# Optimization experiments

Hardware: AMD Instinct MI355X
Metric: run time of the kernel (lower is better)

## Reference

```python
import jax, jax.numpy as jnp
import numpy as np

V, D, C, H = 32, 128, 2048, 8
B, M = 8, 2048
HD = D // H


def rms_norm(x, scale):
    # Whole-tensor (per-batch) RMS over dims (1,2), as in the source (quirky but faithful).
    Bx, Mx, Dx = x.shape
    fr = jnp.sqrt(jnp.sum(x * x, axis=(1, 2))) * (Mx * Dx) ** -0.5  # (B,)
    raw = x / fr[:, None, None]
    return scale[:Mx, :][None, :, :] * raw


def rope_tables(Mx):
    i = jnp.arange(D // 2, dtype=jnp.float32)
    # NOTE: faithful to source: exponent uses (i-1), not i.
    base = jnp.power(10000.0, -2.0 * (i - 1.0) / D)  # (D/2,)
    pos = jnp.arange(Mx, dtype=jnp.float32)
    ang = pos[:, None] * base[None, :]  # (M, D/2)
    return jnp.cos(ang), jnp.sin(ang)


def apply_rope(t, cos, sin):
    # Equivalent to bmm with the block-diagonal 2x2 rotation matrices:
    # out[2i]   =  t[2i]*cos + t[2i+1]*sin
    # out[2i+1] = -t[2i]*sin + t[2i+1]*cos
    te, to = t[..., 0::2], t[..., 1::2]
    oe = te * cos + to * sin
    oo = -te * sin + to * cos
    return jnp.stack([oe, oo], axis=-1).reshape(t.shape)


def mha(q, k, v, in_w, in_b, out_w, out_b):
    Bx, Mx, _ = q.shape
    qp = q @ in_w[:D].T + in_b[:D]
    kp = k @ in_w[D:2 * D].T + in_b[D:2 * D]
    vp = v @ in_w[2 * D:].T + in_b[2 * D:]
    qh = qp.reshape(Bx, Mx, H, HD).transpose(0, 2, 1, 3)
    kh = kp.reshape(Bx, Mx, H, HD).transpose(0, 2, 1, 3)
    vh = vp.reshape(Bx, Mx, H, HD).transpose(0, 2, 1, 3)
    scores = jnp.einsum('bhqd,bhkd->bhqk', qh, kh) / jnp.sqrt(jnp.float32(HD))
    causal = jnp.tril(jnp.ones((Mx, Mx), dtype=bool))
    scores = jnp.where(causal[None, None], scores, -jnp.inf)
    probs = jax.nn.softmax(scores, axis=-1)  # dropout=0.1 in train mode; eval here
    o = jnp.einsum('bhqk,bhkd->bhqd', probs, vh)
    o = o.transpose(0, 2, 1, 3).reshape(Bx, Mx, D)
    return o @ out_w.T + out_b


def setup_inputs():
    key = jax.random.key(0)
    ks = jax.random.split(key, 12)
    s = 0.02
    return {
        'idx': jax.random.randint(ks[0], (B, M), 0, V),
        'targets': jax.random.randint(ks[1], (B, M), 0, V),
        'emb': jax.random.normal(ks[2], (V, D), jnp.float32) * s,
        'rms_scale': jnp.ones((C, D), jnp.float32),
        'Wq': jax.random.normal(ks[3], (D, D), jnp.float32) * s,
        'Wk': jax.random.normal(ks[4], (D, D), jnp.float32) * s,
        'Wv': jax.random.normal(ks[5], (D, D), jnp.float32) * s,
        'in_proj_w': jax.random.normal(ks[6], (3 * D, D), jnp.float32) * s,
        'in_proj_b': jnp.zeros((3 * D,), jnp.float32),
        'out_proj_w': jax.random.normal(ks[7], (D, D), jnp.float32) * s,
        'out_proj_b': jnp.zeros((D,), jnp.float32),
        'lin_w': jax.random.normal(ks[8], (D, D), jnp.float32) * s,
        'lin_b': jnp.zeros((D,), jnp.float32),
        'out_w': jax.random.normal(ks[9], (V, D), jnp.float32) * s,
        'out_b': jnp.zeros((V,), jnp.float32),
    }


def reference(idx, targets, emb, rms_scale, Wq, Wk, Wv, in_proj_w, in_proj_b,
              out_proj_w, out_proj_b, lin_w, lin_b, out_w, out_b):
    x = emb[idx]                                  # (B, M, D)
    x = rms_norm(x, rms_scale)
    Q = x @ Wq.T
    K = x @ Wk.T
    Vv = x @ Wv.T
    cos, sin = rope_tables(x.shape[1])
    q_out = apply_rope(Q, cos, sin)
    k_out = apply_rope(K, cos, sin)
    v_out = apply_rope(Vv, cos, sin)              # source rotates V too (faithful)
    x = x + mha(q_out, k_out, v_out, in_proj_w, in_proj_b, out_proj_w, out_proj_b)
    x = rms_norm(x, rms_scale)
    x = x + jax.nn.relu(x @ lin_w.T + lin_b)
    logits = x @ out_w.T + out_b                  # (B, M, V)
    logp = jax.nn.log_softmax(logits, axis=-1)
    nll = -jnp.take_along_axis(logp, targets[..., None], axis=-1)[..., 0]
    loss = jnp.mean(nll)
    return logits, loss
```

## Files before the change

kernel.cpp:

```cpp
#include <hip/hip_runtime.h>
#include <hip/hip_bf16.h>
#include <math.h>

#define Vv   32
#define Dd   128
#define Hh   8
#define Bb   8
#define Mm   2048
#define BM   (Bb*Mm)
#define NEL  (BM*Dd)
#define XNS  140
#define QKS  396

typedef _Float16 half4_t __attribute__((ext_vector_type(4)));
typedef _Float16 half8_t __attribute__((ext_vector_type(8)));
typedef __fp16   fp16x2  __attribute__((ext_vector_type(2)));
typedef float    float4_t __attribute__((ext_vector_type(4)));
#define MFMA16 __builtin_amdgcn_mfma_f32_16x16x16f16
#define MFMA32 __builtin_amdgcn_mfma_f32_16x16x32_f16

#if __has_builtin(__builtin_amdgcn_exp2f)
__device__ __forceinline__ float fexp2(float x) { return __builtin_amdgcn_exp2f(x); }
#else
__device__ __forceinline__ float fexp2(float x) { return __expf(x * 0.6931471805599453f); }
#endif

__global__ __launch_bounds__(256) void front_kernel(const float* __restrict__ Wq,
                                                    const float* __restrict__ Wk,
                                                    const float* __restrict__ Wv,
                                                    const float* __restrict__ in_w,
                                                    const float* __restrict__ out_pw,
                                                    const float* __restrict__ lin_w,
                                                    const float* __restrict__ out_w,
                                                    _Float16* __restrict__ Wh,
                                                    float* __restrict__ cosT,
                                                    float* __restrict__ sinT,
                                                    const int* __restrict__ idx,
                                                    const float* __restrict__ emb,
                                                    _Float16* __restrict__ Xh,
                                                    float* __restrict__ partials,
                                                    float* __restrict__ lossOut) {
    __shared__ float wsum[4];
    if (blockIdx.x < 1040) {
        if (blockIdx.x == 0 && threadIdx.x == 0) lossOut[0] = 0.f;
        int gid = blockIdx.x * 256 + threadIdx.x;
        if (gid < 135168) {
            const float* src;
            int i;
            if (gid < 131072) {
                int seg = gid >> 14; i = gid & 16383;
                src = seg == 0 ? Wq : seg == 1 ? Wk : seg == 2 ? Wv :
                      seg < 6 ? in_w + (size_t)(seg - 3) * 16384 :
                      seg == 6 ? out_pw : lin_w;
            } else { src = out_w; i = gid - 131072; }
            int tile = i >> 8, within = i & 255;
            int nt = tile >> 3, kk = tile & 7;
            int r = within >> 4, cc = within & 15;
            Wh[gid] = (_Float16)src[(nt * 16 + r) * 128 + kk * 16 + cc];
        } else {
            int rid = gid - 135168;
            int i = rid & 63, m = rid >> 6;
            float ex = -2.0f * ((float)i - 1.0f) / 128.0f;
            float basef = expf(ex * 9.210340371976184f);
            float ang = (float)m * basef;
            cosT[rid] = cosf(ang);
            sinT[rid] = sinf(ang);
        }
    } else {
        int blk = blockIdx.x - 1040;
        int gid = blk * 256 + threadIdx.x;
        int token = gid >> 5, t4 = gid & 31;
        float4 x = *(const float4*)(emb + (size_t)idx[token] * 128 + t4 * 4);
        half4_t o;
        o[0] = (_Float16)x.x; o[1] = (_Float16)x.y; o[2] = (_Float16)x.z; o[3] = (_Float16)x.w;
        *(half4_t*)(Xh + (size_t)gid * 4) = o;
        float v = x.x * x.x + x.y * x.y + x.z * x.z + x.w * x.w;
        #pragma unroll
        for (int off = 32; off; off >>= 1) v += __shfl_xor(v, off);
        int lane = threadIdx.x & 63, wave = threadIdx.x >> 6;
        if (lane == 0) wsum[wave] = v;
        __syncthreads();
        if (threadIdx.x == 0) partials[blk] = wsum[0] + wsum[1] + wsum[2] + wsum[3];
    }
}

__global__ __launch_bounds__(512, 4) void gemm_qkvproj_kernel(const _Float16* __restrict__ xh,
                                                              const float* __restrict__ scale,
                                                              const float* __restrict__ part1,
                                                              const _Float16* __restrict__ Whqkv,
                                                              const _Float16* __restrict__ Whin,
                                                              const float* __restrict__ in_b,
                                                              const float* __restrict__ cosT,
                                                              const float* __restrict__ sinT,
                                                              _Float16* __restrict__ xnh,
                                                              _Float16* __restrict__ Qp,
                                                              _Float16* __restrict__ Kp,
                                                              _Float16* __restrict__ Vp) {
    __shared__ _Float16 xn[32 * XNS];
    __shared__ _Float16 qkv[32 * QKS];
    __shared__ float wsum0[8];
    int tid = threadIdx.x;
    int row0 = blockIdx.x * 32;
    {
        float v = (tid < 256) ? part1[(row0 >> 11) * 256 + tid] : 0.f;
        #pragma unroll
        for (int off = 32; off; off >>= 1) v += __shfl_xor(v, off);
        if ((tid & 63) == 0) wsum0[tid >> 6] = v;
    }
    __syncthreads();
    float iv = 512.0f / sqrtf(((wsum0[0] + wsum0[1]) + (wsum0[2] + wsum0[3])) +
                              ((wsum0[4] + wsum0[5]) + (wsum0[6] + wsum0[7])));
    {
        int rw = tid >> 4, c8 = (tid & 15) * 8;
        int m = (row0 + rw) & (Mm - 1);
        half8_t x8 = *(const half8_t*)(xh + (size_t)(row0 + rw) * 128 + c8);
        const float* sp = scale + (size_t)m * 128 + c8;
        float4 s0 = *(const float4*)sp;
        float4 s1 = *(const float4*)(sp + 4);
        half8_t o8;
        o8[0] = (_Float16)((float)x8[0] * iv * s0.x);
        o8[1] = (_Float16)((float)x8[1] * iv * s0.y);
        o8[2] = (_Float16)((float)x8[2] * iv * s0.z);
        o8[3] = (_Float16)((float)x8[3] * iv * s0.w);
        o8[4] = (_Float16)((float)x8[4] * iv * s1.x);
        o8[5] = (_Float16)((float)x8[5] * iv * s1.y);
        o8[6] = (_Float16)((float)x8[6] * iv * s1.z);
        o8[7] = (_Float16)((float)x8[7] * iv * s1.w);
        *(half8_t*)(xn + rw * XNS + c8) = o8;
        *(half8_t*)(xnh + (size_t)(row0 + rw) * 128 + c8) = o8;
    }
    __syncthreads();
    int wave = tid >> 6, lane = tid & 63;
    int r = lane & 15, c = lane >> 4;
    int nb = wave * 48;
    int aoff = c * 8;
    int boff = r * 16 + (c & 1) * 8;
    int bsel = c >> 1;
    {
        float4_t acc[2][3];
        #pragma unroll
        for (int rt = 0; rt < 2; rt++)
            #pragma unroll
            for (int t = 0; t < 3; t++) acc[rt][t] = (float4_t){0.f, 0.f, 0.f, 0.f};
        #pragma unroll
        for (int kk = 0; kk < 4; kk++) {
            half8_t a0 = *(const half8_t*)(xn + r * XNS + kk * 32 + aoff);
            half8_t a1 = *(const half8_t*)(xn + (16 + r) * XNS + kk * 32 + aoff);
            half8_t wf[3];
            #pragma unroll
            for (int t = 0; t < 3; t++)
                wf[t] = *(const half8_t*)(Whqkv + ((wave * 3 + t) * 8 + kk * 2 + bsel) * 256 + boff);
            #pragma unroll
            for (int t = 0; t < 3; t++) {
                acc[0][t] = MFMA32(a0, wf[t], acc[0][t], 0, 0, 0);
                acc[1][t] = MFMA32(a1, wf[t], acc[1][t], 0, 0, 0);
            }
        }
        #pragma unroll
        for (int rt = 0; rt < 2; rt++) {
            #pragma unroll
            for (int t = 0; t < 3; t++) {
                int n = nb + t * 16 + r;
                int ci = (n & 127) >> 1;
                #pragma unroll
                for (int reg = 0; reg < 4; reg++) {
                    int m2 = (row0 + rt * 16 + 4 * c + reg) & (Mm - 1);
                    float v = acc[rt][t][reg];
                    float vp = __shfl_xor(v, 1);
                    float cs = cosT[m2 * 64 + ci], sn = sinT[m2 * 64 + ci];
                    v = (n & 1) ? (-vp * sn + v * cs) : (v * cs + vp * sn);
                    qkv[(rt * 16 + 4 * c + reg) * QKS + n] = (_Float16)v;
                }
            }
        }
    }
    __syncthreads();
    {
        int seg_lo = nb >> 7;
        int seg_hi = (nb + 32) >> 7;
        float4_t acc[2][3];
        #pragma unroll
        for (int rt = 0; rt < 2; rt++)
            #pragma unroll
            for (int t = 0; t < 3; t++) acc[rt][t] = (float4_t){0.f, 0.f, 0.f, 0.f};
        #pragma unroll
        for (int kk = 0; kk < 4; kk++) {
            half8_t al0 = *(const half8_t*)(qkv + r * QKS + seg_lo * 128 + kk * 32 + aoff);
            half8_t al1 = *(const half8_t*)(qkv + (16 + r) * QKS + seg_lo * 128 + kk * 32 + aoff);
            half8_t ah0 = *(const half8_t*)(qkv + r * QKS + seg_hi * 128 + kk * 32 + aoff);
            half8_t ah1 = *(const half8_t*)(qkv + (16 + r) * QKS + seg_hi * 128 + kk * 32 + aoff);
            #pragma unroll
            for (int t = 0; t < 3; t++) {
                int colg = nb + t * 16;
                int seg = colg >> 7;
                int ntl = (colg & 127) >> 4;
                half8_t wf = *(const half8_t*)(Whin + ((seg * 8 + ntl) * 8 + kk * 2 + bsel) * 256 + boff);
                bool lo = (seg == seg_lo);
                acc[0][t] = MFMA32(lo ? al0 : ah0, wf, acc[0][t], 0, 0, 0);
                acc[1][t] = MFMA32(lo ? al1 : ah1, wf, acc[1][t], 0, 0, 0);
            }
        }
        int bb = row0 >> 11;
        #pragma unroll
        for (int rt = 0; rt < 2; rt++) {
            int t16 = ((row0 + rt * 16) & 2047) >> 4;
            #pragma unroll
            for (int t = 0; t < 3; t++) {
                int colg = nb + t * 16;
                int seg = colg >> 7;
                int h = (colg & 127) >> 4;
                size_t tb = ((size_t)(bb * 8 + h) * 128 + t16) * 256;
                float bv = in_b[colg + r];
                _Float16* dst = seg == 0 ? Qp : seg == 1 ? Kp : Vp;
                #pragma unroll
                for (int reg = 0; reg < 4; reg++) {
                    float v = acc[rt][t][reg] + bv;
                    int key = 4 * c + reg;
                    if (seg < 2) dst[tb + key * 16 + r] = (_Float16)v;
                    else         dst[tb + r * 16 + key] = (_Float16)v;
                }
            }
        }
    }
}

__global__ __launch_bounds__(512, 4) void gemm_ep1_kernel(const _Float16* __restrict__ Oh,
                                                          const _Float16* __restrict__ W6,
                                                          const float* __restrict__ bias,
                                                          const _Float16* __restrict__ xnh,
                                                          _Float16* __restrict__ xresh,
                                                          float* __restrict__ partials) {
    __shared__ _Float16 At[32 * XNS];
    int tid = threadIdx.x;
    int row0 = blockIdx.x * 32;
    {
        int rw = tid >> 4, c8 = (tid & 15) * 8;
        *(half8_t*)(At + rw * XNS + c8) = *(const half8_t*)(Oh + (size_t)(row0 + rw) * 128 + c8);
    }
    __syncthreads();
    int wave = tid >> 6, lane = tid & 63;
    int r = lane & 15, c = lane >> 4;
    int aoff = c * 8;
    int boff = r * 16 + (c & 1) * 8;
    int bsel = c >> 1;
    int n0 = wave * 16;
    float4_t acc[2];
    acc[0] = (float4_t){0.f, 0.f, 0.f, 0.f};
    acc[1] = (float4_t){0.f, 0.f, 0.f, 0.f};
    #pragma unroll
    for (int kk = 0; kk < 4; kk++) {
        half8_t a0 = *(const half8_t*)(At + r * XNS + kk * 32 + aoff);
        half8_t a1 = *(const half8_t*)(At + (16 + r) * XNS + kk * 32 + aoff);
        half8_t wf = *(const half8_t*)(W6 + (wave * 8 + kk * 2 + bsel) * 256 + boff);
        acc[0] = MFMA32(a0, wf, acc[0], 0, 0, 0);
        acc[1] = MFMA32(a1, wf, acc[1], 0, 0, 0);
    }
    float lssq = 0.f;
    int n = n0 + r;
    float bv = bias[n];
    #pragma unroll
    for (int rt = 0; rt < 2; rt++) {
        #pragma unroll
        for (int reg = 0; reg < 4; reg++) {
            int row = row0 + rt * 16 + 4 * c + reg;
            float v = acc[rt][reg] + bv + (float)xnh[(size_t)row * 128 + n];
            lssq += v * v;
            xresh[(size_t)row * 128 + n] = (_Float16)v;
        }
    }
    #pragma unroll
    for (int off = 32; off; off >>= 1) lssq += __shfl_xor(lssq, off);
    __shared__ float wsum[8];
    if (lane == 0) wsum[wave] = lssq;
    __syncthreads();
    if (tid == 0) partials[blockIdx.x] = ((wsum[0] + wsum[1]) + (wsum[2] + wsum[3])) +
                                        ((wsum[4] + wsum[5]) + (wsum[6] + wsum[7]));
}

__global__ __launch_bounds__(512, 4) void gemm_ep2_kernel(const _Float16* __restrict__ xresh,
                                                          const float* __restrict__ scale,
                                                          const float* __restrict__ part2,
                                                          const _Float16* __restrict__ W7,
                                                          const float* __restrict__ bias,
                                                          _Float16* __restrict__ ffoh) {
    __shared__ _Float16 At[32 * XNS];
    int tid = threadIdx.x;
    int row0 = blockIdx.x * 32;
    float pv = part2[(row0 >> 11) * 64 + (tid & 63)];
    #pragma unroll
    for (int off = 32; off; off >>= 1) pv += __shfl_xor(pv, off);
    float iv = 512.0f / sqrtf(pv);
    {
        int rw = tid >> 4, c8 = (tid & 15) * 8;
        int m = (row0 + rw) & (Mm - 1);
        half8_t x8 = *(const half8_t*)(xresh + (size_t)(row0 + rw) * 128 + c8);
        const float* sp = scale + (size_t)m * 128 + c8;
        float4 s0 = *(const float4*)sp;
        float4 s1 = *(const float4*)(sp + 4);
        half8_t o8;
        o8[0] = (_Float16)((float)x8[0] * iv * s0.x);
        o8[1] = (_Float16)((float)x8[1] * iv * s0.y);
        o8[2] = (_Float16)((float)x8[2] * iv * s0.z);
        o8[3] = (_Float16)((float)x8[3] * iv * s0.w);
        o8[4] = (_Float16)((float)x8[4] * iv * s1.x);
        o8[5] = (_Float16)((float)x8[5] * iv * s1.y);
        o8[6] = (_Float16)((float)x8[6] * iv * s1.z);
        o8[7] = (_Float16)((float)x8[7] * iv * s1.w);
        *(half8_t*)(At + rw * XNS + c8) = o8;
    }
    __syncthreads();
    int wave = tid >> 6, lane = tid & 63;
    int r = lane & 15, c = lane >> 4;
    int aoff = c * 8;
    int boff = r * 16 + (c & 1) * 8;
    int bsel = c >> 1;
    int n0 = wave * 16;
    float4_t acc[2];
    acc[0] = (float4_t){0.f, 0.f, 0.f, 0.f};
    acc[1] = (float4_t){0.f, 0.f, 0.f, 0.f};
    #pragma unroll
    for (int kk = 0; kk < 4; kk++) {
        half8_t a0 = *(const half8_t*)(At + r * XNS + kk * 32 + aoff);
        half8_t a1 = *(const half8_t*)(At + (16 + r) * XNS + kk * 32 + aoff);
        half8_t wf = *(const half8_t*)(W7 + (wave * 8 + kk * 2 + bsel) * 256 + boff);
        acc[0] = MFMA32(a0, wf, acc[0], 0, 0, 0);
        acc[1] = MFMA32(a1, wf, acc[1], 0, 0, 0);
    }
    int n = n0 + r;
    float bv = bias[n];
    #pragma unroll
    for (int rt = 0; rt < 2; rt++) {
        #pragma unroll
        for (int reg = 0; reg < 4; reg++) {
            int row = row0 + rt * 16 + 4 * c + reg;
            float v = fmaxf(acc[rt][reg] + bv, 0.f) + (float)xresh[(size_t)row * 128 + n];
            ffoh[(size_t)row * 128 + n] = (_Float16)v;
        }
    }
}

__device__ __forceinline__ half4_t attn_exps(float4_t st, float& ls) {
    float p0 = fexp2(st[0]), p1 = fexp2(st[1]);
    float p2 = fexp2(st[2]), p3 = fexp2(st[3]);
    ls += (p0 + p1) + (p2 + p3);
    fp16x2 lo = __builtin_amdgcn_cvt_pkrtz(p0, p1);
    fp16x2 hi = __builtin_amdgcn_cvt_pkrtz(p2, p3);
    half4_t pf;
    pf[0] = (_Float16)lo[0]; pf[1] = (_Float16)lo[1];
    pf[2] = (_Float16)hi[0]; pf[3] = (_Float16)hi[1];
    return pf;
}
__device__ __forceinline__ half4_t attn_exps_masked(float4_t st, float& ls, int r, int c) {
    float p0 = (4 * c + 0 <= r) ? fexp2(st[0]) : 0.f;
    float p1 = (4 * c + 1 <= r) ? fexp2(st[1]) : 0.f;
    float p2 = (4 * c + 2 <= r) ? fexp2(st[2]) : 0.f;
    float p3 = (4 * c + 3 <= r) ? fexp2(st[3]) : 0.f;
    ls += (p0 + p1) + (p2 + p3);
    fp16x2 lo = __builtin_amdgcn_cvt_pkrtz(p0, p1);
    fp16x2 hi = __builtin_amdgcn_cvt_pkrtz(p2, p3);
    half4_t pf;
    pf[0] = (_Float16)lo[0]; pf[1] = (_Float16)lo[1];
    pf[2] = (_Float16)hi[0]; pf[3] = (_Float16)hi[1];
    return pf;
}

__global__ __launch_bounds__(256) void attn_kernel(const _Float16* __restrict__ Qp,
                                                   const _Float16* __restrict__ Kp,
                                                   const _Float16* __restrict__ Vp,
                                                   _Float16* __restrict__ Oh) {
    __shared__ float mrg[2][10][64];
    int wave = threadIdx.x >> 6, lane = threadIdx.x & 63;
    int pair = blockIdx.x * 2 + (wave >> 1);
    int split = wave & 1;
    int qa = pair & 63, bh = pair >> 6, qb = 127 - qa;
    int r = lane & 15, c = lane >> 4;
    int lofs = r * 16 + 4 * c;
    const _Float16* Kb = Kp + (size_t)bh * 32768 + lofs;
    const _Float16* Vb = Vp + (size_t)bh * 32768 + lofs;
    const _Float16* Qb = Qp + (size_t)bh * 32768 + lofs;
    half4_t qfa = *(const half4_t*)(Qb + qa * 256);
    half4_t qfb = *(const half4_t*)(Qb + qb * 256);
    const _Float16 qscale = (_Float16)0.36067376f;
    qfa *= qscale;
    qfb *= qscale;
    float4_t zero = {0.f, 0.f, 0.f, 0.f};
    float4_t oa = zero, ob = zero;
    float lsa = 0.f, lsb = 0.f;

    for (int kt = split; kt < qa; kt += 2) {
        half4_t k0 = *(const half4_t*)(Kb + (size_t)kt * 256);
        half4_t v0 = *(const half4_t*)(Vb + (size_t)kt * 256);
        float4_t sa = MFMA16(k0, qfa, zero, 0, 0, 0);
        float4_t sb = MFMA16(k0, qfb, zero, 0, 0, 0);
        half4_t pa = attn_exps(sa, lsa);
        half4_t pb = attn_exps(sb, lsb);
        oa = MFMA16(pa, v0, oa, 0, 0, 0);
        ob = MFMA16(pb, v0, ob, 0, 0, 0);
    }
    if ((qa & 1) == split) {
        half4_t k0 = *(const half4_t*)(Kb + (size_t)qa * 256);
        half4_t v0 = *(const half4_t*)(Vb + (size_t)qa * 256);
        float4_t sa = MFMA16(k0, qfa, zero, 0, 0, 0);
        float4_t sb = MFMA16(k0, qfb, zero, 0, 0, 0);
        half4_t pa = attn_exps_masked(sa, lsa, r, c);
        half4_t pb = attn_exps(sb, lsb);
        oa = MFMA16(pa, v0, oa, 0, 0, 0);
        ob = MFMA16(pb, v0, ob, 0, 0, 0);
    }
    {
        int s = qa + 1;
        if ((s & 1) != split) s++;
        for (int kt = s; kt < qb; kt += 2) {
            half4_t k0 = *(const half4_t*)(Kb + (size_t)kt * 256);
            half4_t v0 = *(const half4_t*)(Vb + (size_t)kt * 256);
            float4_t sb = MFMA16(k0, qfb, zero, 0, 0, 0);
            half4_t pb = attn_exps(sb, lsb);
            ob = MFMA16(pb, v0, ob, 0, 0, 0);
        }
    }
    if ((qb & 1) == split) {
        half4_t k0 = *(const half4_t*)(Kb + (size_t)qb * 256);
        half4_t v0 = *(const half4_t*)(Vb + (size_t)qb * 256);
        float4_t sb = MFMA16(k0, qfb, zero, 0, 0, 0);
        half4_t pb = attn_exps_masked(sb, lsb, r, c);
        ob = MFMA16(pb, v0, ob, 0, 0, 0);
    }
    int pib = wave >> 1;
    if (split == 1) {
        #pragma unroll
        for (int i = 0; i < 4; i++) {
            mrg[pib][i][lane] = oa[i];
            mrg[pib][4 + i][lane] = ob[i];
        }
        mrg[pib][8][lane] = lsa;
        mrg[pib][9][lane] = lsb;
    }
    __syncthreads();
    if (split == 0) {
        #pragma unroll
        for (int i = 0; i < 4; i++) {
            oa[i] += mrg[pib][i][lane];
            ob[i] += mrg[pib][4 + i][lane];
        }
        lsa += mrg[pib][8][lane];
        lsb += mrg[pib][9][lane];
        lsa += __shfl_xor(lsa, 16); lsa += __shfl_xor(lsa, 32);
        lsb += __shfl_xor(lsb, 16); lsb += __shfl_xor(lsb, 32);
        int b = bh >> 3, h = bh & 7;
        #pragma unroll
        for (int reg = 0; reg < 4; reg++) {
            float la = __shfl(lsa, 4 * c + reg);
            float lb = __shfl(lsb, 4 * c + reg);
            Oh[(size_t)(b * Mm + qa * 16 + 4 * c + reg) * 128 + h * 16 + r] = (_Float16)(oa[reg] / la);
            Oh[(size_t)(b * Mm + qb * 16 + 4 * c + reg) * 128 + h * 16 + r] = (_Float16)(ob[reg] / lb);
        }
    }
}

__global__ __launch_bounds__(256) void logits_loss_kernel(const _Float16* __restrict__ Xh,
                                                          const _Float16* __restrict__ Wo16,
                                                          const float* __restrict__ bo,
                                                          const int* __restrict__ targets,
                                                          float* __restrict__ logits,
                                                          float* __restrict__ lossOut) {
    __shared__ _Float16 At[64 * XNS];
    __shared__ float wn[4];
    int tid = threadIdx.x;
    int rowb = blockIdx.x * 64;
    #pragma unroll
    for (int it = 0; it < 4; it++) {
        int idx = tid + it * 256;
        int rw = idx >> 4, c8 = (idx & 15) * 8;
        *(half8_t*)(At + rw * XNS + c8) = *(const half8_t*)(Xh + (size_t)(rowb + rw) * 128 + c8);
    }
    __syncthreads();
    int wave = tid >> 6, lane = tid & 63;
    int r = lane & 15, c = lane >> 4;
    int aoff = c * 8;
    int boff = r * 16 + (c & 1) * 8;
    int bsel = c >> 1;
    int row0 = rowb + wave * 16;
    half8_t af[4];
    #pragma unroll
    for (int kk = 0; kk < 4; kk++)
        af[kk] = *(const half8_t*)(At + (wave * 16 + r) * XNS + kk * 32 + aoff);
    float4_t acc[2];
    acc[0] = (float4_t){0.f, 0.f, 0.f, 0.f};
    acc[1] = (float4_t){0.f, 0.f, 0.f, 0.f};
    #pragma unroll
    for (int kk = 0; kk < 4; kk++) {
        #pragma unroll
        for (int t = 0; t < 2; t++) {
            half8_t wf = *(const half8_t*)(Wo16 + (t * 8 + kk * 2 + bsel) * 256 + boff);
            acc[t] = MFMA32(af[kk], wf, acc[t], 0, 0, 0);
        }
    }
    float b0 = bo[r], b1 = bo[r + 16];
    float nll_s = 0.f;
    #pragma unroll
    for (int reg = 0; reg < 4; reg++) {
        int row = row0 + 4 * c + reg;
        float l0 = acc[0][reg] + b0;
        float l1 = acc[1][reg] + b1;
        logits[(size_t)row * 32 + r] = l0;
        logits[(size_t)row * 32 + 16 + r] = l1;
        float mx = fmaxf(l0, l1);
        #pragma unroll
        for (int off = 8; off; off >>= 1) mx = fmaxf(mx, __shfl_xor(mx, off));
        float se = __expf(l0 - mx) + __expf(l1 - mx);
        #pragma unroll
        for (int off = 8; off; off >>= 1) se += __shfl_xor(se, off);
        int tgt = targets[row];
        float sel = (tgt & 16) ? l1 : l0;
        float tval = __shfl(sel, (lane & 48) | (tgt & 15));
        nll_s += logf(se) + mx - tval;
    }
    nll_s += __shfl_xor(nll_s, 16);
    nll_s += __shfl_xor(nll_s, 32);
    if (lane == 0) wn[wave] = nll_s;
    __syncthreads();
    if (tid == 0) atomicAdd(lossOut, ((wn[0] + wn[1]) + (wn[2] + wn[3])) * (1.0f / (float)BM));
}

extern "C" void kernel_launch(void* const* d_in, const int* in_sizes, int n_in,
                              void* d_out, int out_size, void* d_ws, size_t ws_size,
                              hipStream_t stream) {
    const int*   idx       = (const int*)d_in[0];
    const int*   targets   = (const int*)d_in[1];
    const float* emb       = (const float*)d_in[2];
    const float* rms_scale = (const float*)d_in[3];
    const float* Wq        = (const float*)d_in[4];
    const float* Wk        = (const float*)d_in[5];
    const float* Wv        = (const float*)d_in[6];
    const float* in_w      = (const float*)d_in[7];
    const float* in_b      = (const float*)d_in[8];
    const float* out_pw    = (const float*)d_in[9];
    const float* out_pb    = (const float*)d_in[10];
    const float* lin_w     = (const float*)d_in[11];
    const float* lin_b     = (const float*)d_in[12];
    const float* out_w     = (const float*)d_in[13];
    const float* out_b     = (const float*)d_in[14];
    float* out = (float*)d_out;
    float* lossOut = out + (size_t)BM * Vv;

    char* base = (char*)d_ws;
    const size_t MB = 1024 * 1024;
    _Float16* xh16  = (_Float16*)base;
    _Float16* xnh   = (_Float16*)(base + 4 * MB);
    _Float16* Oh    = (_Float16*)(base + 8 * MB);
    _Float16* xresh = (_Float16*)(base + 12 * MB);
    _Float16* ffoh  = (_Float16*)(base + 16 * MB);
    _Float16* Qp    = (_Float16*)(base + 20 * MB);
    _Float16* Kp    = (_Float16*)(base + 24 * MB);
    _Float16* Vp    = (_Float16*)(base + 28 * MB);
    float*    cosT  = (float*)(base + 32 * MB);
    float*    sinT  = cosT + Mm * 64;
    float*    part1 = sinT + Mm * 64;
    float*    part2 = part1 + 2048;
    _Float16* Wh    = (_Float16*)(part2 + 512);

    front_kernel<<<1040 + 2048, 256, 0, stream>>>(Wq, Wk, Wv, in_w, out_pw, lin_w, out_w,
                                                  Wh, cosT, sinT, idx, emb, xh16, part1, lossOut);

    gemm_qkvproj_kernel<<<BM / 32, 512, 0, stream>>>(xh16, rms_scale, part1,
                                                     Wh, Wh + 3 * 16384, in_b,
                                                     cosT, sinT, xnh, Qp, Kp, Vp);

    attn_kernel<<<4096 / 2, 256, 0, stream>>>(Qp, Kp, Vp, Oh);

    gemm_ep1_kernel<<<BM / 32, 512, 0, stream>>>(Oh, Wh + 6 * 16384, out_pb, xnh, xresh, part2);
    gemm_ep2_kernel<<<BM / 32, 512, 0, stream>>>(xresh, rms_scale, part2, Wh + 7 * 16384, lin_b, ffoh);

    logits_loss_kernel<<<BM / 64, 256, 0, stream>>>(ffoh, Wh + 131072, out_b, targets, out, lossOut);
}
```

Measured before the change: 154.6 us.

## Merge all stages into one persistent kernel with software grid barriers

Replaces the six separate launches (front, qkv projection, attention, two epilogue GEMMs, logits/loss) with a single persistent kernel of 256 blocks. The stages are separated by atomic grid-wide barriers, and each block loops over several row tiles. This removes per-launch overhead and the gaps between kernels, and the final loss reduction becomes deterministic instead of using atomics. The cost is lower occupancy and parallelism in each stage, since only 256 blocks are resident. It also relies on all blocks being co-resident, and the barrier has a spin timeout that could silently break ordering.

```diff
diff --git a/kernel.cpp b/kernel.cpp
--- a/kernel.cpp
+++ b/kernel.cpp
@@ -11,6 +11,7 @@
 #define NEL  (BM*Dd)
 #define XNS  140
 #define QKS  396
+#define NBLK 256
 
 typedef _Float16 half4_t __attribute__((ext_vector_type(4)));
 typedef _Float16 half8_t __attribute__((ext_vector_type(8)));
@@ -25,318 +26,29 @@
 __device__ __forceinline__ float fexp2(float x) { return __expf(x * 0.6931471805599453f); }
 #endif
 
-__global__ __launch_bounds__(256) void front_kernel(const float* __restrict__ Wq,
-                                                    const float* __restrict__ Wk,
-                                                    const float* __restrict__ Wv,
-                                                    const float* __restrict__ in_w,
-                                                    const float* __restrict__ out_pw,
-                                                    const float* __restrict__ lin_w,
-                                                    const float* __restrict__ out_w,
-                                                    _Float16* __restrict__ Wh,
-                                                    float* __restrict__ cosT,
-                                                    float* __restrict__ sinT,
-                                                    const int* __restrict__ idx,
-                                                    const float* __restrict__ emb,
-                                                    _Float16* __restrict__ Xh,
-                                                    float* __restrict__ partials,
-                                                    float* __restrict__ lossOut) {
-    __shared__ float wsum[4];
-    if (blockIdx.x < 1040) {
-        if (blockIdx.x == 0 && threadIdx.x == 0) lossOut[0] = 0.f;
-        int gid = blockIdx.x * 256 + threadIdx.x;
-        if (gid < 135168) {
-            const float* src;
-            int i;
-            if (gid < 131072) {
-                int seg = gid >> 14; i = gid & 16383;
-                src = seg == 0 ? Wq : seg == 1 ? Wk : seg == 2 ? Wv :
-                      seg < 6 ? in_w + (size_t)(seg - 3) * 16384 :
-                      seg == 6 ? out_pw : lin_w;
-            } else { src = out_w; i = gid - 131072; }
-            int tile = i >> 8, within = i & 255;
-            int nt = tile >> 3, kk = tile & 7;
-            int r = within >> 4, cc = within & 15;
-            Wh[gid] = (_Float16)src[(nt * 16 + r) * 128 + kk * 16 + cc];
+__device__ __forceinline__ void grid_bar(unsigned* cnt, unsigned* gen) {
+    __syncthreads();
+    if (threadIdx.x == 0) {
+        __threadfence();
+        unsigned g = __hip_atomic_load(gen, __ATOMIC_RELAXED, __HIP_MEMORY_SCOPE_AGENT);
+        unsigned a = __hip_atomic_fetch_add(cnt, 1u, __ATOMIC_ACQ_REL, __HIP_MEMORY_SCOPE_AGENT) + 1u;
+        if (a == (unsigned)NBLK) {
+            __hip_atomic_store(cnt, 0u, __ATOMIC_RELAXED, __HIP_MEMORY_SCOPE_AGENT);
+            __hip_atomic_fetch_add(gen, 1u, __ATOMIC_RELEASE, __HIP_MEMORY_SCOPE_AGENT);
         } else {
-            int rid = gid - 135168;
-            int i = rid & 63, m = rid >> 6;
-            float ex = -2.0f * ((float)i - 1.0f) / 128.0f;
-            float basef = expf(ex * 9.210340371976184f);
-            float ang = (float)m * basef;
-            cosT[rid] = cosf(ang);
-            sinT[rid] = sinf(ang);
-        }
-    } else {
-        int blk = blockIdx.x - 1040;
-        int gid = blk * 256 + threadIdx.x;
-        int token = gid >> 5, t4 = gid & 31;
-        float4 x = *(const float4*)(emb + (size_t)idx[token] * 128 + t4 * 4);
-        half4_t o;
-        o[0] = (_Float16)x.x; o[1] = (_Float16)x.y; o[2] = (_Float16)x.z; o[3] = (_Float16)x.w;
-        *(half4_t*)(Xh + (size_t)gid * 4) = o;
-        float v = x.x * x.x + x.y * x.y + x.z * x.z + x.w * x.w;
-        #pragma unroll
-        for (int off = 32; off; off >>= 1) v += __shfl_xor(v, off);
-        int lane = threadIdx.x & 63, wave = threadIdx.x >> 6;
-        if (lane == 0) wsum[wave] = v;
-        __syncthreads();
-        if (threadIdx.x == 0) partials[blk] = wsum[0] + wsum[1] + wsum[2] + wsum[3];
-    }
+            int spins = 0;
+            while (__hip_atomic_load(gen, __ATOMIC_ACQUIRE, __HIP_MEMORY_SCOPE_AGENT) == g) {
+                __builtin_amdgcn_s_sleep(2);
+                if (++spins > (1 << 19)) break;
+            }
+        }
+        __threadfence();
+    }
+    __syncthreads();
 }
 
-__global__ __launch_bounds__(512, 4) void gemm_qkvproj_kernel(const _Float16* __restrict__ xh,
-                                                              const float* __restrict__ scale,
-                                                              const float* __restrict__ part1,
-                                                              const _Float16* __restrict__ Whqkv,
-                                                              const _Float16* __restrict__ Whin,
-                                                              const float* __restrict__ in_b,
-                                                              const float* __restrict__ cosT,
-                                                              const float* __restrict__ sinT,
-                                                              _Float16* __restrict__ xnh,
-                                                              _Float16* __restrict__ Qp,
-                                                              _Float16* __restrict__ Kp,
-                                                              _Float16* __restrict__ Vp) {
-    __shared__ _Float16 xn[32 * XNS];
-    __shared__ _Float16 qkv[32 * QKS];
-    __shared__ float wsum0[8];
-    int tid = threadIdx.x;
-    int row0 = blockIdx.x * 32;
-    {
-        float v = (tid < 256) ? part1[(row0 >> 11) * 256 + tid] : 0.f;
-        #pragma unroll
-        for (int off = 32; off; off >>= 1) v += __shfl_xor(v, off);
-        if ((tid & 63) == 0) wsum0[tid >> 6] = v;
-    }
-    __syncthreads();
-    float iv = 512.0f / sqrtf(((wsum0[0] + wsum0[1]) + (wsum0[2] + wsum0[3])) +
-                              ((wsum0[4] + wsum0[5]) + (wsum0[6] + wsum0[7])));
-    {
-        int rw = tid >> 4, c8 = (tid & 15) * 8;
-        int m = (row0 + rw) & (Mm - 1);
-        half8_t x8 = *(const half8_t*)(xh + (size_t)(row0 + rw) * 128 + c8);
-        const float* sp = scale + (size_t)m * 128 + c8;
-        float4 s0 = *(const float4*)sp;
-        float4 s1 = *(const float4*)(sp + 4);
-        half8_t o8;
-        o8[0] = (_Float16)((float)x8[0] * iv * s0.x);
-        o8[1] = (_Float16)((float)x8[1] * iv * s0.y);
-        o8[2] = (_Float16)((float)x8[2] * iv * s0.z);
-        o8[3] = (_Float16)((float)x8[3] * iv * s0.w);
-        o8[4] = (_Float16)((float)x8[4] * iv * s1.x);
-        o8[5] = (_Float16)((float)x8[5] * iv * s1.y);
-        o8[6] = (_Float16)((float)x8[6] * iv * s1.z);
-        o8[7] = (_Float16)((float)x8[7] * iv * s1.w);
-        *(half8_t*)(xn + rw * XNS + c8) = o8;
-        *(half8_t*)(xnh + (size_t)(row0 + rw) * 128 + c8) = o8;
-    }
-    __syncthreads();
-    int wave = tid >> 6, lane = tid & 63;
-    int r = lane & 15, c = lane >> 4;
-    int nb = wave * 48;
-    int aoff = c * 8;
-    int boff = r * 16 + (c & 1) * 8;
-    int bsel = c >> 1;
-    {
-        float4_t acc[2][3];
-        #pragma unroll
-        for (int rt = 0; rt < 2; rt++)
-            #pragma unroll
-            for (int t = 0; t < 3; t++) acc[rt][t] = (float4_t){0.f, 0.f, 0.f, 0.f};
-        #pragma unroll
-        for (int kk = 0; kk < 4; kk++) {
-            half8_t a0 = *(const half8_t*)(xn + r * XNS + kk * 32 + aoff);
-            half8_t a1 = *(const half8_t*)(xn + (16 + r) * XNS + kk * 32 + aoff);
-            half8_t wf[3];
-            #pragma unroll
-            for (int t = 0; t < 3; t++)
-                wf[t] = *(const half8_t*)(Whqkv + ((wave * 3 + t) * 8 + kk * 2 + bsel) * 256 + boff);
-            #pragma unroll
-            for (int t = 0; t < 3; t++) {
-                acc[0][t] = MFMA32(a0, wf[t], acc[0][t], 0, 0, 0);
-                acc[1][t] = MFMA32(a1, wf[t], acc[1][t], 0, 0, 0);
-            }
-        }
-        #pragma unroll
-        for (int rt = 0; rt < 2; rt++) {
-            #pragma unroll
-            for (int t = 0; t < 3; t++) {
-                int n = nb + t * 16 + r;
-                int ci = (n & 127) >> 1;
-                #pragma unroll
-                for (int reg = 0; reg < 4; reg++) {
-                    int m2 = (row0 + rt * 16 + 4 * c + reg) & (Mm - 1);
-                    float v = acc[rt][t][reg];
-                    float vp = __shfl_xor(v, 1);
-                    float cs = cosT[m2 * 64 + ci], sn = sinT[m2 * 64 + ci];
-                    v = (n & 1) ? (-vp * sn + v * cs) : (v * cs + vp * sn);
-                    qkv[(rt * 16 + 4 * c + reg) * QKS + n] = (_Float16)v;
-                }
-            }
-        }
-    }
-    __syncthreads();
-    {
-        int seg_lo = nb >> 7;
-        int seg_hi = (nb + 32) >> 7;
-        float4_t acc[2][3];
-        #pragma unroll
-        for (int rt = 0; rt < 2; rt++)
-            #pragma unroll
-            for (int t = 0; t < 3; t++) acc[rt][t] = (float4_t){0.f, 0.f, 0.f, 0.f};
-        #pragma unroll
-        for (int kk = 0; kk < 4; kk++) {
-            half8_t al0 = *(const half8_t*)(qkv + r * QKS + seg_lo * 128 + kk * 32 + aoff);
-            half8_t al1 = *(const half8_t*)(qkv + (16 + r) * QKS + seg_lo * 128 + kk * 32 + aoff);
-            half8_t ah0 = *(const half8_t*)(qkv + r * QKS + seg_hi * 128 + kk * 32 + aoff);
-            half8_t ah1 = *(const half8_t*)(qkv + (16 + r) * QKS + seg_hi * 128 + kk * 32 + aoff);
-            #pragma unroll
-            for (int t = 0; t < 3; t++) {
-                int colg = nb + t * 16;
-                int seg = colg >> 7;
-                int ntl = (colg & 127) >> 4;
-                half8_t wf = *(const half8_t*)(Whin + ((seg * 8 + ntl) * 8 + kk * 2 + bsel) * 256 + boff);
-                bool lo = (seg == seg_lo);
-                acc[0][t] = MFMA32(lo ? al0 : ah0, wf, acc[0][t], 0, 0, 0);
-                acc[1][t] = MFMA32(lo ? al1 : ah1, wf, acc[1][t], 0, 0, 0);
-            }
-        }
-        int bb = row0 >> 11;
-        #pragma unroll
-        for (int rt = 0; rt < 2; rt++) {
-            int t16 = ((row0 + rt * 16) & 2047) >> 4;
-            #pragma unroll
-            for (int t = 0; t < 3; t++) {
-                int colg = nb + t * 16;
-                int seg = colg >> 7;
-                int h = (colg & 127) >> 4;
-                size_t tb = ((size_t)(bb * 8 + h) * 128 + t16) * 256;
-                float bv = in_b[colg + r];
-                _Float16* dst = seg == 0 ? Qp : seg == 1 ? Kp : Vp;
-                #pragma unroll
-                for (int reg = 0; reg < 4; reg++) {
-                    float v = acc[rt][t][reg] + bv;
-                    int key = 4 * c + reg;
-                    if (seg < 2) dst[tb + key * 16 + r] = (_Float16)v;
-                    else         dst[tb + r * 16 + key] = (_Float16)v;
-                }
-            }
-        }
-    }
-}
-
-__global__ __launch_bounds__(512, 4) void gemm_ep1_kernel(const _Float16* __restrict__ Oh,
-                                                          const _Float16* __restrict__ W6,
-                                                          const float* __restrict__ bias,
-                                                          const _Float16* __restrict__ xnh,
-                                                          _Float16* __restrict__ xresh,
-                                                          float* __restrict__ partials) {
-    __shared__ _Float16 At[32 * XNS];
-    int tid = threadIdx.x;
-    int row0 = blockIdx.x * 32;
-    {
-        int rw = tid >> 4, c8 = (tid & 15) * 8;
-        *(half8_t*)(At + rw * XNS + c8) = *(const half8_t*)(Oh + (size_t)(row0 + rw) * 128 + c8);
-    }
-    __syncthreads();
-    int wave = tid >> 6, lane = tid & 63;
-    int r = lane & 15, c = lane >> 4;
-    int aoff = c * 8;
-    int boff = r * 16 + (c & 1) * 8;
-    int bsel = c >> 1;
-    int n0 = wave * 16;
-    float4_t acc[2];
-    acc[0] = (float4_t){0.f, 0.f, 0.f, 0.f};
-    acc[1] = (float4_t){0.f, 0.f, 0.f, 0.f};
-    #pragma unroll
-    for (int kk = 0; kk < 4; kk++) {
-        half8_t a0 = *(const half8_t*)(At + r * XNS + kk * 32 + aoff);
-        half8_t a1 = *(const half8_t*)(At + (16 + r) * XNS + kk * 32 + aoff);
-        half8_t wf = *(const half8_t*)(W6 + (wave * 8 + kk * 2 + bsel) * 256 + boff);
-        acc[0] = MFMA32(a0, wf, acc[0], 0, 0, 0);
-        acc[1] = MFMA32(a1, wf, acc[1], 0, 0, 0);
-    }
-    float lssq = 0.f;
-    int n = n0 + r;
-    float bv = bias[n];
-    #pragma unroll
-    for (int rt = 0; rt < 2; rt++) {
-        #pragma unroll
-        for (int reg = 0; reg < 4; reg++) {
-            int row = row0 + rt * 16 + 4 * c + reg;
-            float v = acc[rt][reg] + bv + (float)xnh[(size_t)row * 128 + n];
-            lssq += v * v;
-            xresh[(size_t)row * 128 + n] = (_Float16)v;
-        }
-    }
-    #pragma unroll
-    for (int off = 32; off; off >>= 1) lssq += __shfl_xor(lssq, off);
-    __shared__ float wsum[8];
-    if (lane == 0) wsum[wave] = lssq;
-    __syncthreads();
-    if (tid == 0) partials[blockIdx.x] = ((wsum[0] + wsum[1]) + (wsum[2] + wsum[3])) +
-                                        ((wsum[4] + wsum[5]) + (wsum[6] + wsum[7]));
-}
-
-__global__ __launch_bounds__(512, 4) void gemm_ep2_kernel(const _Float16* __restrict__ xresh,
-                                                          const float* __restrict__ scale,
-                                                          const float* __restrict__ part2,
-                                                          const _Float16* __restrict__ W7,
-                                                          const float* __restrict__ bias,
-                                                          _Float16* __restrict__ ffoh) {
-    __shared__ _Float16 At[32 * XNS];
-    int tid = threadIdx.x;
-    int row0 = blockIdx.x * 32;
-    float pv = part2[(row0 >> 11) * 64 + (tid & 63)];
-    #pragma unroll
-    for (int off = 32; off; off >>= 1) pv += __shfl_xor(pv, off);
-    float iv = 512.0f / sqrtf(pv);
-    {
-        int rw = tid >> 4, c8 = (tid & 15) * 8;
-        int m = (row0 + rw) & (Mm - 1);
-        half8_t x8 = *(const half8_t*)(xresh + (size_t)(row0 + rw) * 128 + c8);
-        const float* sp = scale + (size_t)m * 128 + c8;
-        float4 s0 = *(const float4*)sp;
-        float4 s1 = *(const float4*)(sp + 4);
-        half8_t o8;
-        o8[0] = (_Float16)((float)x8[0] * iv * s0.x);
-        o8[1] = (_Float16)((float)x8[1] * iv * s0.y);
-        o8[2] = (_Float16)((float)x8[2] * iv * s0.z);
-        o8[3] = (_Float16)((float)x8[3] * iv * s0.w);
-        o8[4] = (_Float16)((float)x8[4] * iv * s1.x);
-        o8[5] = (_Float16)((float)x8[5] * iv * s1.y);
-        o8[6] = (_Float16)((float)x8[6] * iv * s1.z);
-        o8[7] = (_Float16)((float)x8[7] * iv * s1.w);
-        *(half8_t*)(At + rw * XNS + c8) = o8;
-    }
-    __syncthreads();
-    int wave = tid >> 6, lane = tid & 63;
-    int r = lane & 15, c = lane >> 4;
-    int aoff = c * 8;
-    int boff = r * 16 + (c & 1) * 8;
-    int bsel = c >> 1;
-    int n0 = wave * 16;
-    float4_t acc[2];
-    acc[0] = (float4_t){0.f, 0.f, 0.f, 0.f};
-    acc[1] = (float4_t){0.f, 0.f, 0.f, 0.f};
-    #pragma unroll
-    for (int kk = 0; kk < 4; kk++) {
-        half8_t a0 = *(const half8_t*)(At + r * XNS + kk * 32 + aoff);
-        half8_t a1 = *(const half8_t*)(At + (16 + r) * XNS + kk * 32 + aoff);
-        half8_t wf = *(const half8_t*)(W7 + (wave * 8 + kk * 2 + bsel) * 256 + boff);
-        acc[0] = MFMA32(a0, wf, acc[0], 0, 0, 0);
-        acc[1] = MFMA32(a1, wf, acc[1], 0, 0, 0);
-    }
-    int n = n0 + r;
-    float bv = bias[n];
-    #pragma unroll
-    for (int rt = 0; rt < 2; rt++) {
-        #pragma unroll
-        for (int reg = 0; reg < 4; reg++) {
-            int row = row0 + rt * 16 + 4 * c + reg;
-            float v = fmaxf(acc[rt][reg] + bv, 0.f) + (float)xresh[(size_t)row * 128 + n];
-            ffoh[(size_t)row * 128 + n] = (_Float16)v;
-        }
-    }
+__global__ __launch_bounds__(64) void init_kernel(unsigned* __restrict__ bar) {
+    bar[threadIdx.x] = 0u;
 }
 
 __device__ __forceinline__ half4_t attn_exps(float4_t st, float& ls) {
@@ -364,162 +76,489 @@
     return pf;
 }
 
-__global__ __launch_bounds__(256) void attn_kernel(const _Float16* __restrict__ Qp,
-                                                   const _Float16* __restrict__ Kp,
-                                                   const _Float16* __restrict__ Vp,
-                                                   _Float16* __restrict__ Oh) {
-    __shared__ float mrg[2][10][64];
-    int wave = threadIdx.x >> 6, lane = threadIdx.x & 63;
-    int pair = blockIdx.x * 2 + (wave >> 1);
-    int split = wave & 1;
-    int qa = pair & 63, bh = pair >> 6, qb = 127 - qa;
-    int r = lane & 15, c = lane >> 4;
-    int lofs = r * 16 + 4 * c;
-    const _Float16* Kb = Kp + (size_t)bh * 32768 + lofs;
-    const _Float16* Vb = Vp + (size_t)bh * 32768 + lofs;
-    const _Float16* Qb = Qp + (size_t)bh * 32768 + lofs;
-    half4_t qfa = *(const half4_t*)(Qb + qa * 256);
-    half4_t qfb = *(const half4_t*)(Qb + qb * 256);
-    const _Float16 qscale = (_Float16)0.36067376f;
-    qfa *= qscale;
-    qfb *= qscale;
-    float4_t zero = {0.f, 0.f, 0.f, 0.f};
-    float4_t oa = zero, ob = zero;
-    float lsa = 0.f, lsb = 0.f;
-
-    for (int kt = split; kt < qa; kt += 2) {
-        half4_t k0 = *(const half4_t*)(Kb + (size_t)kt * 256);
-        half4_t v0 = *(const half4_t*)(Vb + (size_t)kt * 256);
-        float4_t sa = MFMA16(k0, qfa, zero, 0, 0, 0);
-        float4_t sb = MFMA16(k0, qfb, zero, 0, 0, 0);
-        half4_t pa = attn_exps(sa, lsa);
-        half4_t pb = attn_exps(sb, lsb);
-        oa = MFMA16(pa, v0, oa, 0, 0, 0);
-        ob = MFMA16(pb, v0, ob, 0, 0, 0);
-    }
-    if ((qa & 1) == split) {
-        half4_t k0 = *(const half4_t*)(Kb + (size_t)qa * 256);
-        half4_t v0 = *(const half4_t*)(Vb + (size_t)qa * 256);
-        float4_t sa = MFMA16(k0, qfa, zero, 0, 0, 0);
-        float4_t sb = MFMA16(k0, qfb, zero, 0, 0, 0);
-        half4_t pa = attn_exps_masked(sa, lsa, r, c);
-        half4_t pb = attn_exps(sb, lsb);
-        oa = MFMA16(pa, v0, oa, 0, 0, 0);
-        ob = MFMA16(pb, v0, ob, 0, 0, 0);
-    }
-    {
-        int s = qa + 1;
-        if ((s & 1) != split) s++;
-        for (int kt = s; kt < qb; kt += 2) {
-            half4_t k0 = *(const half4_t*)(Kb + (size_t)kt * 256);
-            half4_t v0 = *(const half4_t*)(Vb + (size_t)kt * 256);
-            float4_t sb = MFMA16(k0, qfb, zero, 0, 0, 0);
-            half4_t pb = attn_exps(sb, lsb);
-            ob = MFMA16(pb, v0, ob, 0, 0, 0);
-        }
-    }
-    if ((qb & 1) == split) {
-        half4_t k0 = *(const half4_t*)(Kb + (size_t)qb * 256);
-        half4_t v0 = *(const half4_t*)(Vb + (size_t)qb * 256);
-        float4_t sb = MFMA16(k0, qfb, zero, 0, 0, 0);
-        half4_t pb = attn_exps_masked(sb, lsb, r, c);
-        ob = MFMA16(pb, v0, ob, 0, 0, 0);
-    }
-    int pib = wave >> 1;
-    if (split == 1) {
-        #pragma unroll
-        for (int i = 0; i < 4; i++) {
-            mrg[pib][i][lane] = oa[i];
-            mrg[pib][4 + i][lane] = ob[i];
-        }
-        mrg[pib][8][lane] = lsa;
-        mrg[pib][9][lane] = lsb;
-    }
-    __syncthreads();
-    if (split == 0) {
-        #pragma unroll
-        for (int i = 0; i < 4; i++) {
-            oa[i] += mrg[pib][i][lane];
-            ob[i] += mrg[pib][4 + i][lane];
-        }
-        lsa += mrg[pib][8][lane];
-        lsb += mrg[pib][9][lane];
-        lsa += __shfl_xor(lsa, 16); lsa += __shfl_xor(lsa, 32);
-        lsb += __shfl_xor(lsb, 16); lsb += __shfl_xor(lsb, 32);
-        int b = bh >> 3, h = bh & 7;
-        #pragma unroll
-        for (int reg = 0; reg < 4; reg++) {
-            float la = __shfl(lsa, 4 * c + reg);
-            float lb = __shfl(lsb, 4 * c + reg);
-            Oh[(size_t)(b * Mm + qa * 16 + 4 * c + reg) * 128 + h * 16 + r] = (_Float16)(oa[reg] / la);
-            Oh[(size_t)(b * Mm + qb * 16 + 4 * c + reg) * 128 + h * 16 + r] = (_Float16)(ob[reg] / lb);
-        }
-    }
-}
-
-__global__ __launch_bounds__(256) void logits_loss_kernel(const _Float16* __restrict__ Xh,
-                                                          const _Float16* __restrict__ Wo16,
-                                                          const float* __restrict__ bo,
-                                                          const int* __restrict__ targets,
-                                                          float* __restrict__ logits,
-                                                          float* __restrict__ lossOut) {
-    __shared__ _Float16 At[64 * XNS];
-    __shared__ float wn[4];
-    int tid = threadIdx.x;
-    int rowb = blockIdx.x * 64;
-    #pragma unroll
-    for (int it = 0; it < 4; it++) {
-        int idx = tid + it * 256;
-        int rw = idx >> 4, c8 = (idx & 15) * 8;
-        *(half8_t*)(At + rw * XNS + c8) = *(const half8_t*)(Xh + (size_t)(rowb + rw) * 128 + c8);
-    }
-    __syncthreads();
+__global__ __launch_bounds__(512, 4) void mega_kernel(
+    const int*   __restrict__ idx,
+    const int*   __restrict__ targets,
+    const float* __restrict__ emb,
+    const float* __restrict__ scale,
+    const float* __restrict__ Wq,
+    const float* __restrict__ Wk,
+    const float* __restrict__ Wv,
+    const float* __restrict__ in_w,
+    const float* __restrict__ in_b,
+    const float* __restrict__ out_pw,
+    const float* __restrict__ out_pb,
+    const float* __restrict__ lin_w,
+    const float* __restrict__ lin_b,
+    const float* __restrict__ out_w,
+    const float* __restrict__ out_b,
+    char* __restrict__ ws,
+    float* __restrict__ out)
+{
+    const size_t MB = 1024 * 1024;
+    _Float16* xh16  = (_Float16*)ws;
+    _Float16* xnh   = (_Float16*)(ws + 4 * MB);
+    _Float16* Oh    = (_Float16*)(ws + 8 * MB);
+    _Float16* xresh = (_Float16*)(ws + 12 * MB);
+    _Float16* ffoh  = (_Float16*)(ws + 16 * MB);
+    _Float16* Qp    = (_Float16*)(ws + 20 * MB);
+    _Float16* Kp    = (_Float16*)(ws + 24 * MB);
+    _Float16* Vp    = (_Float16*)(ws + 28 * MB);
+    float*    cosT  = (float*)(ws + 32 * MB);
+    float*    sinT  = cosT + Mm * 64;
+    float*    part1 = sinT + Mm * 64;
+    float*    part2 = part1 + 2048;
+    _Float16* Wh    = (_Float16*)(part2 + 512);
+    unsigned* cnt   = (unsigned*)(ws + 40 * MB);
+    unsigned* gen   = (unsigned*)(ws + 40 * MB) + 32;
+    float*    nllPart = (float*)(ws + 40 * MB + 4096);
+    float*    lossOut = out + (size_t)BM * Vv;
+    float*    logits  = out;
+
+    __shared__ union SH {
+        struct { _Float16 xn[32 * XNS]; _Float16 qkv[32 * QKS]; float wsum[8]; } b;
+        struct { float mrg[4][10][64]; } c;
+        struct { _Float16 At[128 * XNS]; float wn[8]; } f;
+        struct { float wsum[8]; } a;
+    } sh;
+
+    int tid  = threadIdx.x;
+    int bid  = blockIdx.x;
     int wave = tid >> 6, lane = tid & 63;
     int r = lane & 15, c = lane >> 4;
     int aoff = c * 8;
     int boff = r * 16 + (c & 1) * 8;
     int bsel = c >> 1;
-    int row0 = rowb + wave * 16;
-    half8_t af[4];
-    #pragma unroll
-    for (int kk = 0; kk < 4; kk++)
-        af[kk] = *(const half8_t*)(At + (wave * 16 + r) * XNS + kk * 32 + aoff);
-    float4_t acc[2];
-    acc[0] = (float4_t){0.f, 0.f, 0.f, 0.f};
-    acc[1] = (float4_t){0.f, 0.f, 0.f, 0.f};
-    #pragma unroll
-    for (int kk = 0; kk < 4; kk++) {
-        #pragma unroll
-        for (int t = 0; t < 2; t++) {
-            half8_t wf = *(const half8_t*)(Wo16 + (t * 8 + kk * 2 + bsel) * 256 + boff);
-            acc[t] = MFMA32(af[kk], wf, acc[t], 0, 0, 0);
-        }
-    }
-    float b0 = bo[r], b1 = bo[r + 16];
-    float nll_s = 0.f;
-    #pragma unroll
-    for (int reg = 0; reg < 4; reg++) {
-        int row = row0 + 4 * c + reg;
-        float l0 = acc[0][reg] + b0;
-        float l1 = acc[1][reg] + b1;
-        logits[(size_t)row * 32 + r] = l0;
-        logits[(size_t)row * 32 + 16 + r] = l1;
-        float mx = fmaxf(l0, l1);
-        #pragma unroll
-        for (int off = 8; off; off >>= 1) mx = fmaxf(mx, __shfl_xor(mx, off));
-        float se = __expf(l0 - mx) + __expf(l1 - mx);
-        #pragma unroll
-        for (int off = 8; off; off >>= 1) se += __shfl_xor(se, off);
-        int tgt = targets[row];
-        float sel = (tgt & 16) ? l1 : l0;
-        float tval = __shfl(sel, (lane & 48) | (tgt & 15));
-        nll_s += logf(se) + mx - tval;
-    }
-    nll_s += __shfl_xor(nll_s, 16);
-    nll_s += __shfl_xor(nll_s, 32);
-    if (lane == 0) wn[wave] = nll_s;
-    __syncthreads();
-    if (tid == 0) atomicAdd(lossOut, ((wn[0] + wn[1]) + (wn[2] + wn[3])) * (1.0f / (float)BM));
+
+    #pragma unroll 1
+    for (int sweep = 0; sweep < 3; sweep++) {
+        int gid = sweep * 131072 + bid * 512 + tid;
+        if (gid < 135168) {
+            const float* src;
+            int i;
+            if (gid < 131072) {
+                int seg = gid >> 14; i = gid & 16383;
+                src = seg == 0 ? Wq : seg == 1 ? Wk : seg == 2 ? Wv :
+                      seg < 6 ? in_w + (size_t)(seg - 3) * 16384 :
+                      seg == 6 ? out_pw : lin_w;
+            } else { src = out_w; i = gid - 131072; }
+            int tile = i >> 8, within = i & 255;
+            int nt = tile >> 3, kk = tile & 7;
+            int rr = within >> 4, cc = within & 15;
+            Wh[gid] = (_Float16)src[(nt * 16 + rr) * 128 + kk * 16 + cc];
+        } else if (gid < 266240) {
+            int rid = gid - 135168;
+            int i = rid & 63, m = rid >> 6;
+            float ex = -2.0f * ((float)i - 1.0f) / 128.0f;
+            float basef = expf(ex * 9.210340371976184f);
+            float ang = (float)m * basef;
+            cosT[rid] = cosf(ang);
+            sinT[rid] = sinf(ang);
+        }
+    }
+    #pragma unroll 1
+    for (int pass = 0; pass < 4; pass++) {
+        int chunk = pass * 256 + bid;
+        int slot = chunk * 512 + tid;
+        int token = slot >> 5, t4 = slot & 31;
+        float4 x = *(const float4*)(emb + (size_t)idx[token] * 128 + t4 * 4);
+        half4_t o;
+        o[0] = (_Float16)x.x; o[1] = (_Float16)x.y; o[2] = (_Float16)x.z; o[3] = (_Float16)x.w;
+        *(half4_t*)(xh16 + (size_t)slot * 4) = o;
+        float v = x.x * x.x + x.y * x.y + x.z * x.z + x.w * x.w;
+        #pragma unroll
+        for (int off = 32; off; off >>= 1) v += __shfl_xor(v, off);
+        __syncthreads();
+        if (lane == 0) sh.a.wsum[wave] = v;
+        __syncthreads();
+        if (tid == 0)
+            part1[chunk] = ((sh.a.wsum[0] + sh.a.wsum[1]) + (sh.a.wsum[2] + sh.a.wsum[3])) +
+                           ((sh.a.wsum[4] + sh.a.wsum[5]) + (sh.a.wsum[6] + sh.a.wsum[7]));
+    }
+    grid_bar(cnt, gen);
+
+    #pragma unroll 1
+    for (int it = 0; it < 2; it++) {
+        int row0 = (bid + it * 256) * 32;
+        __syncthreads();
+        {
+            float v = (tid < 128) ? part1[(row0 >> 11) * 128 + tid] : 0.f;
+            #pragma unroll
+            for (int off = 32; off; off >>= 1) v += __shfl_xor(v, off);
+            if ((tid & 63) == 0) sh.b.wsum[tid >> 6] = v;
+        }
+        __syncthreads();
+        float iv = 512.0f / sqrtf(((sh.b.wsum[0] + sh.b.wsum[1]) + (sh.b.wsum[2] + sh.b.wsum[3])) +
+                                  ((sh.b.wsum[4] + sh.b.wsum[5]) + (sh.b.wsum[6] + sh.b.wsum[7])));
+        {
+            int rw = tid >> 4, c8 = (tid & 15) * 8;
+            int m = (row0 + rw) & (Mm - 1);
+            half8_t x8 = *(const half8_t*)(xh16 + (size_t)(row0 + rw) * 128 + c8);
+            const float* sp = scale + (size_t)m * 128 + c8;
+            float4 s0 = *(const float4*)sp;
+            float4 s1 = *(const float4*)(sp + 4);
+            half8_t o8;
+            o8[0] = (_Float16)((float)x8[0] * iv * s0.x);
+            o8[1] = (_Float16)((float)x8[1] * iv * s0.y);
+            o8[2] = (_Float16)((float)x8[2] * iv * s0.z);
+            o8[3] = (_Float16)((float)x8[3] * iv * s0.w);
+            o8[4] = (_Float16)((float)x8[4] * iv * s1.x);
+            o8[5] = (_Float16)((float)x8[5] * iv * s1.y);
+            o8[6] = (_Float16)((float)x8[6] * iv * s1.z);
+            o8[7] = (_Float16)((float)x8[7] * iv * s1.w);
+            *(half8_t*)(sh.b.xn + rw * XNS + c8) = o8;
+            *(half8_t*)(xnh + (size_t)(row0 + rw) * 128 + c8) = o8;
+        }
+        __syncthreads();
+        int nb = wave * 48;
+        {
+            float4_t acc[2][3];
+            #pragma unroll
+            for (int rt = 0; rt < 2; rt++)
+                #pragma unroll
+                for (int t = 0; t < 3; t++) acc[rt][t] = (float4_t){0.f, 0.f, 0.f, 0.f};
+            #pragma unroll
+            for (int kk = 0; kk < 4; kk++) {
+                half8_t a0 = *(const half8_t*)(sh.b.xn + r * XNS + kk * 32 + aoff);
+                half8_t a1 = *(const half8_t*)(sh.b.xn + (16 + r) * XNS + kk * 32 + aoff);
+                half8_t wf[3];
+                #pragma unroll
+                for (int t = 0; t < 3; t++)
+                    wf[t] = *(const half8_t*)(Wh + ((wave * 3 + t) * 8 + kk * 2 + bsel) * 256 + boff);
+                #pragma unroll
+                for (int t = 0; t < 3; t++) {
+                    acc[0][t] = MFMA32(a0, wf[t], acc[0][t], 0, 0, 0);
+                    acc[1][t] = MFMA32(a1, wf[t], acc[1][t], 0, 0, 0);
+                }
+            }
+            #pragma unroll
+            for (int rt = 0; rt < 2; rt++) {
+                #pragma unroll
+                for (int t = 0; t < 3; t++) {
+                    int n = nb + t * 16 + r;
+                    int ci = (n & 127) >> 1;
+                    #pragma unroll
+                    for (int reg = 0; reg < 4; reg++) {
+                        int m2 = (row0 + rt * 16 + 4 * c + reg) & (Mm - 1);
+                        float v = acc[rt][t][reg];
+                        float vp = __shfl_xor(v, 1);
+                        float cs = cosT[m2 * 64 + ci], sn = sinT[m2 * 64 + ci];
+                        v = (n & 1) ? (-vp * sn + v * cs) : (v * cs + vp * sn);
+                        sh.b.qkv[(rt * 16 + 4 * c + reg) * QKS + n] = (_Float16)v;
+                    }
+                }
+            }
+        }
+        __syncthreads();
+        {
+            const _Float16* Whin = Wh + 3 * 16384;
+            int seg_lo = nb >> 7;
+            int seg_hi = (nb + 32) >> 7;
+            float4_t acc[2][3];
+            #pragma unroll
+            for (int rt = 0; rt < 2; rt++)
+                #pragma unroll
+                for (int t = 0; t < 3; t++) acc[rt][t] = (float4_t){0.f, 0.f, 0.f, 0.f};
+            #pragma unroll
+            for (int kk = 0; kk < 4; kk++) {
+                half8_t al0 = *(const half8_t*)(sh.b.qkv + r * QKS + seg_lo * 128 + kk * 32 + aoff);
+                half8_t al1 = *(const half8_t*)(sh.b.qkv + (16 + r) * QKS + seg_lo * 128 + kk * 32 + aoff);
+                half8_t ah0 = *(const half8_t*)(sh.b.qkv + r * QKS + seg_hi * 128 + kk * 32 + aoff);
+                half8_t ah1 = *(const half8_t*)(sh.b.qkv + (16 + r) * QKS + seg_hi * 128 + kk * 32 + aoff);
+                #pragma unroll
+                for (int t = 0; t < 3; t++) {
+                    int colg = nb + t * 16;
+                    int seg = colg >> 7;
+                    int ntl = (colg & 127) >> 4;
+                    half8_t wf = *(const half8_t*)(Whin + ((seg * 8 + ntl) * 8 + kk * 2 + bsel) * 256 + boff);
+                    bool lo = (seg == seg_lo);
+                    acc[0][t] = MFMA32(lo ? al0 : ah0, wf, acc[0][t], 0, 0, 0);
+                    acc[1][t] = MFMA32(lo ? al1 : ah1, wf, acc[1][t], 0, 0, 0);
+                }
+            }
+            int bb = row0 >> 11;
+            #pragma unroll
+            for (int rt = 0; rt < 2; rt++) {
+                int t16 = ((row0 + rt * 16) & 2047) >> 4;
+                #pragma unroll
+                for (int t = 0; t < 3; t++) {
+                    int colg = nb + t * 16;
+                    int seg = colg >> 7;
+                    int h = (colg & 127) >> 4;
+                    size_t tb = ((size_t)(bb * 8 + h) * 128 + t16) * 256;
+                    float bv = in_b[colg + r];
+                    _Float16* dst = seg == 0 ? Qp : seg == 1 ? Kp : Vp;
+                    #pragma unroll
+                    for (int reg = 0; reg < 4; reg++) {
+                        float v = acc[rt][t][reg] + bv;
+                        int key = 4 * c + reg;
+                        if (seg < 2) dst[tb + key * 16 + r] = (_Float16)v;
+                        else         dst[tb + r * 16 + key] = (_Float16)v;
+                    }
+                }
+            }
+        }
+    }
+    grid_bar(cnt, gen);
+
+    {
+        int lofs = r * 16 + 4 * c;
+        const _Float16 qscale = (_Float16)0.36067376f;
+        #pragma unroll 1
+        for (int pass = 0; pass < 4; pass++) {
+            int pair = pass * 1024 + bid * 4 + (wave >> 1);
+            int split = wave & 1;
+            int qa = pair & 63, bh = pair >> 6, qb = 127 - qa;
+            const _Float16* Kb = Kp + (size_t)bh * 32768 + lofs;
+            const _Float16* Vb = Vp + (size_t)bh * 32768 + lofs;
+            const _Float16* Qb = Qp + (size_t)bh * 32768 + lofs;
+            half4_t qfa = *(const half4_t*)(Qb + qa * 256);
+            half4_t qfb = *(const half4_t*)(Qb + qb * 256);
+            qfa *= qscale;
+            qfb *= qscale;
+            float4_t zero = {0.f, 0.f, 0.f, 0.f};
+            float4_t oa = zero, ob = zero;
+            float lsa = 0.f, lsb = 0.f;
+
+            for (int kt = split; kt < qa; kt += 2) {
+                half4_t k0 = *(const half4_t*)(Kb + (size_t)kt * 256);
+                half4_t v0 = *(const half4_t*)(Vb + (size_t)kt * 256);
+                float4_t sa = MFMA16(k0, qfa, zero, 0, 0, 0);
+                float4_t sb = MFMA16(k0, qfb, zero, 0, 0, 0);
+                half4_t pa = attn_exps(sa, lsa);
+                half4_t pb = attn_exps(sb, lsb);
+                oa = MFMA16(pa, v0, oa, 0, 0, 0);
+                ob = MFMA16(pb, v0, ob, 0, 0, 0);
+            }
+            if ((qa & 1) == split) {
+                half4_t k0 = *(const half4_t*)(Kb + (size_t)qa * 256);
+                half4_t v0 = *(const half4_t*)(Vb + (size_t)qa * 256);
+                float4_t sa = MFMA16(k0, qfa, zero, 0, 0, 0);
+                float4_t sb = MFMA16(k0, qfb, zero, 0, 0, 0);
+                half4_t pa = attn_exps_masked(sa, lsa, r, c);
+                half4_t pb = attn_exps(sb, lsb);
+                oa = MFMA16(pa, v0, oa, 0, 0, 0);
+                ob = MFMA16(pb, v0, ob, 0, 0, 0);
+            }
+            {
+                int s = qa + 1;
+                if ((s & 1) != split) s++;
+                for (int kt = s; kt < qb; kt += 2) {
+                    half4_t k0 = *(const half4_t*)(Kb + (size_t)kt * 256);
+                    half4_t v0 = *(const half4_t*)(Vb + (size_t)kt * 256);
+                    float4_t sb = MFMA16(k0, qfb, zero, 0, 0, 0);
+                    half4_t pb = attn_exps(sb, lsb);
+                    ob = MFMA16(pb, v0, ob, 0, 0, 0);
+                }
+            }
+            if ((qb & 1) == split) {
+                half4_t k0 = *(const half4_t*)(Kb + (size_t)qb * 256);
+                half4_t v0 = *(const half4_t*)(Vb + (size_t)qb * 256);
+                float4_t sb = MFMA16(k0, qfb, zero, 0, 0, 0);
+                half4_t pb = attn_exps_masked(sb, lsb, r, c);
+                ob = MFMA16(pb, v0, ob, 0, 0, 0);
+            }
+            int pib = wave >> 1;
+            __syncthreads();
+            if (split == 1) {
+                #pragma unroll
+                for (int i = 0; i < 4; i++) {
+                    sh.c.mrg[pib][i][lane] = oa[i];
+                    sh.c.mrg[pib][4 + i][lane] = ob[i];
+                }
+                sh.c.mrg[pib][8][lane] = lsa;
+                sh.c.mrg[pib][9][lane] = lsb;
+            }
+            __syncthreads();
+            if (split == 0) {
+                #pragma unroll
+                for (int i = 0; i < 4; i++) {
+                    oa[i] += sh.c.mrg[pib][i][lane];
+                    ob[i] += sh.c.mrg[pib][4 + i][lane];
+                }
+                lsa += sh.c.mrg[pib][8][lane];
+                lsb += sh.c.mrg[pib][9][lane];
+                lsa += __shfl_xor(lsa, 16); lsa += __shfl_xor(lsa, 32);
+                lsb += __shfl_xor(lsb, 16); lsb += __shfl_xor(lsb, 32);
+                int b = bh >> 3, h = bh & 7;
+                #pragma unroll
+                for (int reg = 0; reg < 4; reg++) {
+                    float la = __shfl(lsa, 4 * c + reg);
+                    float lb = __shfl(lsb, 4 * c + reg);
+                    Oh[(size_t)(b * Mm + qa * 16 + 4 * c + reg) * 128 + h * 16 + r] = (_Float16)(oa[reg] / la);
+                    Oh[(size_t)(b * Mm + qb * 16 + 4 * c + reg) * 128 + h * 16 + r] = (_Float16)(ob[reg] / lb);
+                }
+            }
+        }
+    }
+    grid_bar(cnt, gen);
+
+    #pragma unroll 1
+    for (int it = 0; it < 2; it++) {
+        int rg = bid + it * 256;
+        int row0 = rg * 32;
+        __syncthreads();
+        const _Float16* W6 = Wh + 6 * 16384;
+        {
+            int rw = tid >> 4, c8 = (tid & 15) * 8;
+            *(half8_t*)(sh.f.At + rw * XNS + c8) = *(const half8_t*)(Oh + (size_t)(row0 + rw) * 128 + c8);
+        }
+        __syncthreads();
+        int n0 = wave * 16;
+        float4_t acc[2];
+        acc[0] = (float4_t){0.f, 0.f, 0.f, 0.f};
+        acc[1] = (float4_t){0.f, 0.f, 0.f, 0.f};
+        #pragma unroll
+        for (int kk = 0; kk < 4; kk++) {
+            half8_t a0 = *(const half8_t*)(sh.f.At + r * XNS + kk * 32 + aoff);
+            half8_t a1 = *(const half8_t*)(sh.f.At + (16 + r) * XNS + kk * 32 + aoff);
+            half8_t wf = *(const half8_t*)(W6 + (wave * 8 + kk * 2 + bsel) * 256 + boff);
+            acc[0] = MFMA32(a0, wf, acc[0], 0, 0, 0);
+            acc[1] = MFMA32(a1, wf, acc[1], 0, 0, 0);
+        }
+        float lssq = 0.f;
+        int n = n0 + r;
+        float bv = out_pb[n];
+        #pragma unroll
+        for (int rt = 0; rt < 2; rt++) {
+            #pragma unroll
+            for (int reg = 0; reg < 4; reg++) {
+                int row = row0 + rt * 16 + 4 * c + reg;
+                float v = acc[rt][reg] + bv + (float)xnh[(size_t)row * 128 + n];
+                lssq += v * v;
+                xresh[(size_t)row * 128 + n] = (_Float16)v;
+            }
+        }
+        #pragma unroll
+        for (int off = 32; off; off >>= 1) lssq += __shfl_xor(lssq, off);
+        if (lane == 0) sh.f.wn[wave] = lssq;
+        __syncthreads();
+        if (tid == 0) part2[rg] = ((sh.f.wn[0] + sh.f.wn[1]) + (sh.f.wn[2] + sh.f.wn[3])) +
+                                  ((sh.f.wn[4] + sh.f.wn[5]) + (sh.f.wn[6] + sh.f.wn[7]));
+    }
+    grid_bar(cnt, gen);
+
+    #pragma unroll 1
+    for (int it = 0; it < 2; it++) {
+        int row0 = (bid + it * 256) * 32;
+        const _Float16* W7 = Wh + 7 * 16384;
+        float pv = part2[(row0 >> 11) * 64 + (tid & 63)];
+        #pragma unroll
+        for (int off = 32; off; off >>= 1) pv += __shfl_xor(pv, off);
+        float iv = 512.0f / sqrtf(pv);
+        __syncthreads();
+        {
+            int rw = tid >> 4, c8 = (tid & 15) * 8;
+            int m = (row0 + rw) & (Mm - 1);
+            half8_t x8 = *(const half8_t*)(xresh + (size_t)(row0 + rw) * 128 + c8);
+            const float* sp = scale + (size_t)m * 128 + c8;
+            float4 s0 = *(const float4*)sp;
+            float4 s1 = *(const float4*)(sp + 4);
+            half8_t o8;
+            o8[0] = (_Float16)((float)x8[0] * iv * s0.x);
+            o8[1] = (_Float16)((float)x8[1] * iv * s0.y);
+            o8[2] = (_Float16)((float)x8[2] * iv * s0.z);
+            o8[3] = (_Float16)((float)x8[3] * iv * s0.w);
+            o8[4] = (_Float16)((float)x8[4] * iv * s1.x);
+            o8[5] = (_Float16)((float)x8[5] * iv * s1.y);
+            o8[6] = (_Float16)((float)x8[6] * iv * s1.z);
+            o8[7] = (_Float16)((float)x8[7] * iv * s1.w);
+            *(half8_t*)(sh.f.At + rw * XNS + c8) = o8;
+        }
+        __syncthreads();
+        int n0 = wave * 16;
+        float4_t acc[2];
+        acc[0] = (float4_t){0.f, 0.f, 0.f, 0.f};
+        acc[1] = (float4_t){0.f, 0.f, 0.f, 0.f};
+        #pragma unroll
+        for (int kk = 0; kk < 4; kk++) {
+            half8_t a0 = *(const half8_t*)(sh.f.At + r * XNS + kk * 32 + aoff);
+            half8_t a1 = *(const half8_t*)(sh.f.At + (16 + r) * XNS + kk * 32 + aoff);
+            half8_t wf = *(const half8_t*)(W7 + (wave * 8 + kk * 2 + bsel) * 256 + boff);
+            acc[0] = MFMA32(a0, wf, acc[0], 0, 0, 0);
+            acc[1] = MFMA32(a1, wf, acc[1], 0, 0, 0);
+        }
+        int n = n0 + r;
+        float bv = lin_b[n];
+        #pragma unroll
+        for (int rt = 0; rt < 2; rt++) {
+            #pragma unroll
+            for (int reg = 0; reg < 4; reg++) {
+                int row = row0 + rt * 16 + 4 * c + reg;
+                float v = fmaxf(acc[rt][reg] + bv, 0.f) + (float)xresh[(size_t)row * 128 + n];
+                ffoh[(size_t)row * 128 + n] = (_Float16)v;
+            }
+        }
+    }
+    grid_bar(cnt, gen);
+
+    if (bid < 128) {
+        const _Float16* Wo16 = Wh + 131072;
+        int rowb = bid * 128;
+        #pragma unroll
+        for (int it = 0; it < 4; it++) {
+            int idx2 = tid + it * 512;
+            int rw = idx2 >> 4, c8 = (idx2 & 15) * 8;
+            *(half8_t*)(sh.f.At + rw * XNS + c8) = *(const half8_t*)(ffoh + (size_t)(rowb + rw) * 128 + c8);
+        }
+        __syncthreads();
+        int row0 = rowb + wave * 16;
+        half8_t af[4];
+        #pragma unroll
+        for (int kk = 0; kk < 4; kk++)
+            af[kk] = *(const half8_t*)(sh.f.At + (wave * 16 + r) * XNS + kk * 32 + aoff);
+        float4_t acc[2];
+        acc[0] = (float4_t){0.f, 0.f, 0.f, 0.f};
+        acc[1] = (float4_t){0.f, 0.f, 0.f, 0.f};
+        #pragma unroll
+        for (int kk = 0; kk < 4; kk++) {
+            #pragma unroll
+            for (int t = 0; t < 2; t++) {
+                half8_t wf = *(const half8_t*)(Wo16 + (t * 8 + kk * 2 + bsel) * 256 + boff);
+                acc[t] = MFMA32(af[kk], wf, acc[t], 0, 0, 0);
+            }
+        }
+        float b0 = out_b[r], b1 = out_b[r + 16];
+        float nll_s = 0.f;
+        #pragma unroll
+        for (int reg = 0; reg < 4; reg++) {
+            int row = row0 + 4 * c + reg;
+            float l0 = acc[0][reg] + b0;
+            float l1 = acc[1][reg] + b1;
+            logits[(size_t)row * 32 + r] = l0;
+            logits[(size_t)row * 32 + 16 + r] = l1;
+            float mx = fmaxf(l0, l1);
+            #pragma unroll
+            for (int off = 8; off; off >>= 1) mx = fmaxf(mx, __shfl_xor(mx, off));
+            float se = __expf(l0 - mx) + __expf(l1 - mx);
+            #pragma unroll
+            for (int off = 8; off; off >>= 1) se += __shfl_xor(se, off);
+            int tgt = targets[row];
+            float sel = (tgt & 16) ? l1 : l0;
+            float tval = __shfl(sel, (lane & 48) | (tgt & 15));
+            nll_s += logf(se) + mx - tval;
+        }
+        nll_s += __shfl_xor(nll_s, 16);
+        nll_s += __shfl_xor(nll_s, 32);
+        if (lane == 0) sh.f.wn[wave] = nll_s;
+        __syncthreads();
+        if (tid == 0)
+            nllPart[bid] = ((sh.f.wn[0] + sh.f.wn[1]) + (sh.f.wn[2] + sh.f.wn[3])) +
+                           ((sh.f.wn[4] + sh.f.wn[5]) + (sh.f.wn[6] + sh.f.wn[7]));
+    }
+    grid_bar(cnt, gen);
+
+    if (bid == 0) {
+        float v = (tid < 128) ? nllPart[tid] : 0.f;
+        #pragma unroll
+        for (int off = 32; off; off >>= 1) v += __shfl_xor(v, off);
+        __syncthreads();
+        if (lane == 0) sh.a.wsum[wave] = v;
+        __syncthreads();
+        if (tid == 0)
+            lossOut[0] = (((sh.a.wsum[0] + sh.a.wsum[1]) + (sh.a.wsum[2] + sh.a.wsum[3])) +
+                          ((sh.a.wsum[4] + sh.a.wsum[5]) + (sh.a.wsum[6] + sh.a.wsum[7]))) * (1.0f / (float)BM);
+    }
 }
 
 extern "C" void kernel_launch(void* const* d_in, const int* in_sizes, int n_in,
@@ -540,36 +579,13 @@
     const float* lin_b     = (const float*)d_in[12];
     const float* out_w     = (const float*)d_in[13];
     const float* out_b     = (const float*)d_in[14];
+    char* ws  = (char*)d_ws;
     float* out = (float*)d_out;
-    float* lossOut = out + (size_t)BM * Vv;
-
-    char* base = (char*)d_ws;
-    const size_t MB = 1024 * 1024;
-    _Float16* xh16  = (_Float16*)base;
-    _Float16* xnh   = (_Float16*)(base + 4 * MB);
-    _Float16* Oh    = (_Float16*)(base + 8 * MB);
-    _Float16* xresh = (_Float16*)(base + 12 * MB);
-    _Float16* ffoh  = (_Float16*)(base + 16 * MB);
-    _Float16* Qp    = (_Float16*)(base + 20 * MB);
-    _Float16* Kp    = (_Float16*)(base + 24 * MB);
-    _Float16* Vp    = (_Float16*)(base + 28 * MB);
-    float*    cosT  = (float*)(base + 32 * MB);
-    float*    sinT  = cosT + Mm * 64;
-    float*    part1 = sinT + Mm * 64;
-    float*    part2 = part1 + 2048;
-    _Float16* Wh    = (_Float16*)(part2 + 512);
-
-    front_kernel<<<1040 + 2048, 256, 0, stream>>>(Wq, Wk, Wv, in_w, out_pw, lin_w, out_w,
-                                                  Wh, cosT, sinT, idx, emb, xh16, part1, lossOut);
-
-    gemm_qkvproj_kernel<<<BM / 32, 512, 0, stream>>>(xh16, rms_scale, part1,
-                                                     Wh, Wh + 3 * 16384, in_b,
-                                                     cosT, sinT, xnh, Qp, Kp, Vp);
-
-    attn_kernel<<<4096 / 2, 256, 0, stream>>>(Qp, Kp, Vp, Oh);
-
-    gemm_ep1_kernel<<<BM / 32, 512, 0, stream>>>(Oh, Wh + 6 * 16384, out_pb, xnh, xresh, part2);
-    gemm_ep2_kernel<<<BM / 32, 512, 0, stream>>>(xresh, rms_scale, part2, Wh + 7 * 16384, lin_b, ffoh);
-
-    logits_loss_kernel<<<BM / 64, 256, 0, stream>>>(ffoh, Wh + 131072, out_b, targets, out, lossOut);
+    unsigned* bar = (unsigned*)(ws + 40 * 1024 * 1024);
+
+    init_kernel<<<1, 64, 0, stream>>>(bar);
+    mega_kernel<<<NBLK, 512, 0, stream>>>(idx, targets, emb, rms_scale,
+                                          Wq, Wk, Wv, in_w, in_b,
+                                          out_pw, out_pb, lin_w, lin_b,
+                                          out_w, out_b, ws, out);
 }
```

After: 409.4 us. 2.65x slower.
